# Performance work log

Measured on AMD Instinct MI355X. Metric: run time of the kernel, lower is better.

## Reference

```python
import jax, jax.numpy as jnp
import numpy as np

VOC, EMB, HID = 32000, 512, 1024
B, S = 16, 256


def setup_inputs() -> dict:
    key = jax.random.key(0)
    ks = jax.random.split(key, 12)
    s_e = 1.0 / np.sqrt(HID)
    inp = {
        "inputs": jax.random.randint(ks[0], (B, S), 0, VOC, dtype=jnp.int64),
        "emb": jax.random.normal(ks[1], (VOC, EMB), dtype=jnp.float32),
        "W_ih1": jax.random.uniform(ks[2], (4 * HID, EMB), minval=-s_e, maxval=s_e),
        "W_hh1": jax.random.uniform(ks[3], (4 * HID, HID), minval=-s_e, maxval=s_e),
        "b_ih1": jax.random.uniform(ks[4], (4 * HID,), minval=-s_e, maxval=s_e),
        "b_hh1": jax.random.uniform(ks[5], (4 * HID,), minval=-s_e, maxval=s_e),
        "W_ih2": jax.random.uniform(ks[6], (4 * HID, HID), minval=-s_e, maxval=s_e),
        "W_hh2": jax.random.uniform(ks[7], (4 * HID, HID), minval=-s_e, maxval=s_e),
        "b_ih2": jax.random.uniform(ks[8], (4 * HID,), minval=-s_e, maxval=s_e),
        "b_hh2": jax.random.uniform(ks[9], (4 * HID,), minval=-s_e, maxval=s_e),
        "W_log": jax.random.uniform(ks[10], (VOC, HID), minval=-s_e, maxval=s_e),
        "b_log": jnp.zeros((VOC,), dtype=jnp.float32),  # init_weights zeroes logits bias
    }
    return inp


def _lstm_cell(x, h, c, W_ih, W_hh, b_ih, b_hh):
    # PyTorch LSTMCell: gates ordered (i, f, g, o)
    g = x @ W_ih.T + b_ih + h @ W_hh.T + b_hh  # [B, 4H]
    i, f, gg, o = jnp.split(g, 4, axis=-1)
    c_new = jax.nn.sigmoid(f) * c + jax.nn.sigmoid(i) * jnp.tanh(gg)
    h_new = jax.nn.sigmoid(o) * jnp.tanh(c_new)
    return h_new, c_new


def reference(inputs, emb, W_ih1, W_hh1, b_ih1, b_hh1,
              W_ih2, W_hh2, b_ih2, b_hh2, W_log, b_log):
    # Dropout is evaluated in inference mode (identity), for determinism.
    embed = emb[inputs]  # [B, S, E]
    xs = jnp.swapaxes(embed, 0, 1)  # [S, B, E]
    bsz = inputs.shape[0]
    h1 = jnp.zeros((bsz, HID), embed.dtype)
    c1 = jnp.zeros((bsz, HID), embed.dtype)
    h2 = jnp.zeros((bsz, HID), embed.dtype)
    c2 = jnp.zeros((bsz, HID), embed.dtype)

    def step(carry, x_t):
        h1, c1, h2, c2 = carry
        h1, c1 = _lstm_cell(x_t, h1, c1, W_ih1, W_hh1, b_ih1, b_hh1)
        h2, c2 = _lstm_cell(h1, h2, c2, W_ih2, W_hh2, b_ih2, b_hh2)
        return (h1, c1, h2, c2), h2

    _, hid_seq = jax.lax.scan(step, (h1, c1, h2, c2), xs)  # [S, B, H]
    hid_seq = jnp.swapaxes(hid_seq, 0, 1)  # [B, S, H]
    logits = hid_seq @ W_log.T + b_log  # [B, S, V]
    return jax.nn.log_softmax(logits, axis=-1)
```

## Files before the change

kernel.cpp:

```cpp
#include <hip/hip_runtime.h>
#include <hip/hip_bf16.h>

typedef __attribute__((ext_vector_type(8))) _Float16 half8;
typedef __attribute__((ext_vector_type(4))) _Float16 half4;
typedef __attribute__((ext_vector_type(4))) float f32x4;
typedef __attribute__((ext_vector_type(4))) unsigned int u32x4;

#define VOC 32000
#define EMB 512
#define HID 1024
#define SS  256
#define NROW 4096
#define CHK 43
#define CSTRIDE 64
#define SLOTB (64 * CSTRIDE * 16)
#define NS 4
#define SPIN (1 << 16)
#define ROWH 264

__device__ __forceinline__ float sigf(float x) {
    return 1.f / (1.f + __expf(-x));
}
__device__ __forceinline__ float tanh_c(float x) {
    x = fminf(fmaxf(x, -15.f), 15.f);
    float e = __expf(2.f * x);
    return (e - 1.f) / (e + 1.f);
}

__device__ __forceinline__ u32x4 ldg_u4_cc(const void* p) {
    u32x4 r;
    asm volatile("global_load_dwordx4 %0, %1, off sc0 sc1" : "=v"(r) : "v"(p));
    return r;
}
__device__ __forceinline__ void stg_u4_cc(void* p, u32x4 v) {
    asm volatile("global_store_dwordx4 %0, %1, off sc0 sc1" :: "v"(p), "v"(v) : "memory");
}
__device__ __forceinline__ void stg_u32_cc(unsigned* p, unsigned v) {
    asm volatile("global_store_dword %0, %1, off sc0 sc1" :: "v"(p), "v"(v) : "memory");
}
__device__ __forceinline__ unsigned ldg_u32_cc(const unsigned* p) {
    unsigned v;
    asm volatile("global_load_dword %0, %1, off sc0 sc1\n\ts_waitcnt vmcnt(0)"
                 : "=v"(v) : "v"(p) : "memory");
    return v;
}
__device__ __forceinline__ half8 to_agpr(half8 v) {
    asm volatile("" : "+a"(v));
    return v;
}
__device__ __forceinline__ void gload16(const void* g, void* lds) {
    __builtin_amdgcn_global_load_lds(
        (const __attribute__((address_space(1))) unsigned int*)(uintptr_t)g,
        (__attribute__((address_space(3))) unsigned int*)(unsigned int)(uintptr_t)lds,
        16, 0, 0);
}

__global__ void k_zero(float* p, int n) {
    int i = blockIdx.x * blockDim.x + threadIdx.x;
    int st = gridDim.x * blockDim.x;
    for (; i < n; i += st) p[i] = 0.f;
}

__global__ void k_cvt_all(const float* __restrict__ s0, const float* __restrict__ s1,
                          const float* __restrict__ s2, const float* __restrict__ s3,
                          const float* __restrict__ s4,
                          _Float16* __restrict__ d0, _Float16* __restrict__ d1,
                          _Float16* __restrict__ d2, _Float16* __restrict__ d3,
                          _Float16* __restrict__ d4) {
    const int n0 = 4096 * 512 / 4;
    const int n1 = 4096 * 1024 / 4;
    const int n4 = VOC * 1024 / 4;
    const int nT = n0 + 3 * n1 + n4;
    int i = blockIdx.x * 256 + threadIdx.x;
    int st = gridDim.x * 256;
    for (; i < nT; i += st) {
        const float* s; _Float16* d; int k = i;
        if (k < n0) { s = s0; d = d0; }
        else {
            k -= n0;
            if (k < n1) { s = s1; d = d1; }
            else {
                k -= n1;
                if (k < n1) { s = s2; d = d2; }
                else {
                    k -= n1;
                    if (k < n1) { s = s3; d = d3; }
                    else { k -= n1; s = s4; d = d4; }
                }
            }
        }
        float4 v = ((const float4*)s)[k];
        half4 o = {(_Float16)v.x, (_Float16)v.y, (_Float16)v.z, (_Float16)v.w};
        ((half4*)d)[k] = o;
    }
}

__global__ void k_bias(const float* bi1, const float* bh1,
                       const float* bi2, const float* bh2,
                       float* b1, float* b2) {
    int i = blockIdx.x * blockDim.x + threadIdx.x;
    if (i < 4 * HID) { b1[i] = bi1[i] + bh1[i]; b2[i] = bi2[i] + bh2[i]; }
}

__global__ void k_embed(const int* __restrict__ tok, const float* __restrict__ emb,
                        _Float16* __restrict__ A) {
    int idx = blockIdx.x * 256 + threadIdx.x;
    if (idx >= NROW * (EMB / 4)) return;
    int r = idx >> 7, c4 = idx & 127;
    int t = r >> 4, b = r & 15;
    int token = tok[b * SS + t];
    float4 v = ((const float4*)(emb + (size_t)token * EMB))[c4];
    half4 o = {(_Float16)v.x, (_Float16)v.y, (_Float16)v.z, (_Float16)v.w};
    ((half4*)(A + (size_t)r * EMB))[c4] = o;
}

template <int F16OUT>
__global__ __launch_bounds__(256) void k_gemm_bt(
    const _Float16* __restrict__ A, const _Float16* __restrict__ B,
    const float* __restrict__ bias, float* __restrict__ C,
    _Float16* __restrict__ Ch, int M, int N, int K, int scatter, int swz) {
    __shared__ __align__(16) _Float16 As[128 * 32];
    __shared__ __align__(16) _Float16 Bs[128 * 32];
    int tid = threadIdx.x;
    int wave = tid >> 6, lane = tid & 63;
    int nbx = gridDim.x;
    int lin = blockIdx.y * nbx + blockIdx.x;
    if (swz) {
        int n = nbx * gridDim.y, cpx = n >> 3;
        lin = (lin & 7) * cpx + (lin >> 3);
    }
    int bRow = (lin / nbx) * 128, bCol = (lin % nbx) * 128;
    int wr = (wave >> 1) * 64, wc = (wave & 1) * 64;
    f32x4 acc[4][4] = {};

    int lrow = lane & 15, khalf = (lane >> 4) * 8;

    for (int kt = 0; kt < K; kt += 32) {
#pragma unroll
        for (int q = 0; q < 2; ++q) {
            int ci = q * 256 + wave * 64 + lane;
            int row = ci >> 2, c8 = (ci & 3) * 8;
            int ldsoff = (q * 256 + wave * 64) * 16;
            gload16(A + (size_t)(bRow + row) * K + kt + c8, (char*)As + ldsoff);
            gload16(B + (size_t)(bCol + row) * K + kt + c8, (char*)Bs + ldsoff);
        }
        __syncthreads();
        half8 a[4], b[4];
#pragma unroll
        for (int i = 0; i < 4; ++i)
            a[i] = *(const half8*)(&As[(wr + 16 * i + lrow) * 32 + khalf]);
#pragma unroll
        for (int j = 0; j < 4; ++j)
            b[j] = *(const half8*)(&Bs[(wc + 16 * j + lrow) * 32 + khalf]);
#pragma unroll
        for (int i = 0; i < 4; ++i)
#pragma unroll
            for (int j = 0; j < 4; ++j)
                acc[i][j] = __builtin_amdgcn_mfma_f32_16x16x32_f16(a[i], b[j], acc[i][j], 0, 0, 0);
        __syncthreads();
    }

    int lcol = lane & 15, lrow4 = (lane >> 4) * 4;
#pragma unroll
    for (int i = 0; i < 4; ++i)
#pragma unroll
        for (int j = 0; j < 4; ++j)
#pragma unroll
            for (int q = 0; q < 4; ++q) {
                int gr = bRow + wr + 16 * i + lrow4 + q;
                int gc = bCol + wc + 16 * j + lcol;
                float v = acc[i][j][q] + bias[gc];
                size_t orow = scatter ? (size_t)(((gr & 15) << 8) | (gr >> 4)) : (size_t)gr;
                if (F16OUT) Ch[orow * (size_t)N + gc] = (_Float16)v;
                else        C[orow * (size_t)N + gc] = v;
            }
}

template <int F16OUT>
__global__ __launch_bounds__(512, 1) void k_gemm8(
    const _Float16* __restrict__ A, const _Float16* __restrict__ B,
    const float* __restrict__ bias, float* __restrict__ Cf,
    _Float16* __restrict__ Ch, int M, int N, int K, int scatter) {
    __shared__ __align__(16) char smem[131072];
    int tid = threadIdx.x;
    int wave = tid >> 6, lane = tid & 63;
    int wm = wave >> 2, wn = wave & 3;
    int nbx = gridDim.x;
    int lin = blockIdx.y * nbx + blockIdx.x;
    {
        int n = nbx * gridDim.y;
        if ((n & 7) == 0) { int cpx = n >> 3; lin = (lin & 7) * cpx + (lin >> 3); }
    }
    int bRow = (lin / nbx) * 256, bCol = (lin % nbx) * 256;
    int nt = K >> 6;
    int lrow = lane & 15, kq = lane >> 4;

    auto stage = [&](int mat, int h, int t) {
        const _Float16* src = mat ? B : A;
        int r0 = mat ? bCol : bRow;
        char* dst = smem + (size_t)(t & 1) * 65536 + mat * 32768 + h * 16384;
#pragma unroll
        for (int j = 0; j < 2; ++j) {
            int ci = j * 512 + tid;
            int row = ci >> 3, slot = ci & 7;
            int grow = h * 128 + row;
            int gsl = slot ^ (row & 7);
            gload16(src + (size_t)(r0 + grow) * K + t * 64 + gsl * 8, dst + ci * 16);
        }
    };
    auto rdA = [&](int bf, int mi, int kk) -> half8 {
        int r = wm * 128 + mi * 16 + lrow;
        int sl = (kk * 4 + kq) ^ (lrow & 7);
        return *(const half8*)(smem + (size_t)bf * 65536 + r * 128 + sl * 16);
    };
    auto rdB = [&](int bf, int ni, int kk) -> half8 {
        int r = wn * 64 + ni * 16 + lrow;
        int sl = (kk * 4 + kq) ^ (lrow & 7);
        return *(const half8*)(smem + (size_t)bf * 65536 + 32768 + r * 128 + sl * 16);
    };

    f32x4 acc[8][4] = {};

    stage(1, 0, 0); stage(0, 0, 0); stage(1, 1, 0); stage(0, 1, 0);
    if (nt > 1) { stage(1, 0, 1); stage(0, 0, 1); }

    for (int u = 0; u < nt; ++u) {
        int bf = u & 1;
        if (u + 1 == nt) asm volatile("s_waitcnt vmcnt(0)" ::: "memory");
        else             asm volatile("s_waitcnt vmcnt(4)" ::: "memory");
        __builtin_amdgcn_s_barrier();
        __builtin_amdgcn_sched_barrier(0);
        if (u + 1 < nt) stage(1, 1, u + 1);
        half8 a[8][2], b[4][2];
#pragma unroll
        for (int mi = 0; mi < 8; ++mi)
#pragma unroll
            for (int kk = 0; kk < 2; ++kk)
                a[mi][kk] = rdA(bf, mi, kk);
#pragma unroll
        for (int ni = 0; ni < 4; ++ni)
#pragma unroll
            for (int kk = 0; kk < 2; ++kk)
                b[ni][kk] = rdB(bf, ni, kk);
        __builtin_amdgcn_s_setprio(1);
#pragma unroll
        for (int mi = 0; mi < 8; ++mi)
#pragma unroll
            for (int ni = 0; ni < 4; ++ni) {
                acc[mi][ni] = __builtin_amdgcn_mfma_f32_16x16x32_f16(a[mi][0], b[ni][0], acc[mi][ni], 0, 0, 0);
                acc[mi][ni] = __builtin_amdgcn_mfma_f32_16x16x32_f16(a[mi][1], b[ni][1], acc[mi][ni], 0, 0, 0);
            }
        __builtin_amdgcn_s_setprio(0);
        asm volatile("s_waitcnt lgkmcnt(0)" ::: "memory");
        __builtin_amdgcn_s_barrier();
        __builtin_amdgcn_sched_barrier(0);
        if (u + 1 < nt) stage(0, 1, u + 1);
        if (u + 2 < nt) { stage(1, 0, u + 2); stage(0, 0, u + 2); }
    }

    float bv[4];
#pragma unroll
    for (int ni = 0; ni < 4; ++ni)
        bv[ni] = bias[bCol + wn * 64 + ni * 16 + lrow];
#pragma unroll
    for (int mi = 0; mi < 8; ++mi)
#pragma unroll
        for (int ni = 0; ni < 4; ++ni)
#pragma unroll
            for (int q = 0; q < 4; ++q) {
                int gr = bRow + wm * 128 + mi * 16 + kq * 4 + q;
                int gc = bCol + wn * 64 + ni * 16 + lrow;
                float v = acc[mi][ni][q] + bv[ni];
                size_t orow = scatter ? (size_t)(((gr & 15) << 8) | (gr >> 4)) : (size_t)gr;
                if (F16OUT) Ch[orow * (size_t)N + gc] = (_Float16)v;
                else        Cf[orow * (size_t)N + gc] = v;
            }
}

__device__ __forceinline__ void poll_stage2(const char* base, int exp, int cnt,
                                            unsigned short* hs, int sbp, int r) {
    u32x4 cv[11];
#pragma unroll
    for (int j = 0; j < 11; ++j)
        if (j < cnt) cv[j] = ldg_u4_cc(base + j * 64);
    for (int it = 0; it < SPIN; ++it) {
        asm volatile("s_waitcnt vmcnt(0)" ::: "memory");
        __builtin_amdgcn_sched_barrier(0);
        bool bad = false;
#pragma unroll
        for (int j = 0; j < 11; ++j)
            if (j < cnt && (int)cv[j][3] < exp) {
                cv[j] = ldg_u4_cc(base + j * 64);
                bad = true;
            }
        if (!bad) break;
        __builtin_amdgcn_s_sleep(1);
    }
#pragma unroll
    for (int j = 0; j < 11; ++j)
        if (j < cnt) {
            int c = r + 4 * j;
            unsigned* dst = (unsigned*)((char*)hs + sbp * (2 * ROWH) + c * 12);
            dst[0] = cv[j][0]; dst[1] = cv[j][1]; dst[2] = cv[j][2];
        }
}

__global__ __launch_bounds__(256, 1) void k_rnn(
    const _Float16* __restrict__ X,
    const _Float16* __restrict__ Whh1,
    const _Float16* __restrict__ Wih2,
    const _Float16* __restrict__ Whh2,
    const float* __restrict__ b2s,
    char* __restrict__ h1buf,
    char* __restrict__ h2buf,
    unsigned* __restrict__ prog,
    _Float16* __restrict__ h2seq) {
    __shared__ __align__(16) unsigned short hsPA[64 * ROWH];
    __shared__ __align__(16) unsigned short hsPB[64 * ROWH];
    __shared__ float gs[4][1024];
    __shared__ __align__(16) unsigned short hstage[264];
    int tid = threadIdx.x;
    int w = tid >> 6, l = tid & 63;
    int bid = blockIdx.x;
    int layer = bid >> 6, sb = bid & 63;
    int sbp = tid >> 2, r = tid & 3;
    int cnt = (r == 3) ? 10 : 11;
    size_t choff = (size_t)(sbp * CSTRIDE + r) * 16;
    int hp = l >> 5;
    int hoff = (l & 15) * 16 + ((l >> 4) & 1) * 8;

    half8 wA[32];
    half8 wB[32];
    {
        const _Float16* base = layer ? Wih2 : Whh1;
        const _Float16* wp = base + (size_t)(w * HID + sb * 16 + (l & 15)) * HID + (l >> 4) * 8;
#pragma unroll
        for (int kt = 0; kt < 32; ++kt)
            wA[kt] = to_agpr(*(const half8*)(wp + kt * 32));
        if (layer) {
            const _Float16* wq = Whh2 + (size_t)(w * HID + sb * 16 + (l & 15)) * HID + (l >> 4) * 8;
#pragma unroll
            for (int kt = 0; kt < 32; ++kt)
                wB[kt] = to_agpr(*(const half8*)(wq + kt * 32));
        }
    }
    float bias_v = layer ? b2s[w * HID + sb * 16 + (l & 15)] : 0.f;

    int eb = tid >> 4, ecol = tid & 15;
    int gidx = ((eb >> 2) * 16 + ecol) * 4 + (eb & 3);
    float creg = 0.f;
    int pc = 0;

    if (!layer) {
        const _Float16* xbase = X + (size_t)w * HID + sb * 16 + (l & 15);
        int bq = (l >> 4) * 4;
        f32x4 xreg;
        {
            const _Float16* xp = xbase + (size_t)bq * 4096;
            xreg[0] = (float)xp[0]; xreg[1] = (float)xp[4096];
            xreg[2] = (float)xp[8192]; xreg[3] = (float)xp[12288];
        }
        for (int g = 0; g < SS; ++g) {
            int tn = (g + 1 < SS) ? g + 1 : SS - 1;
            const _Float16* xp = xbase + (size_t)(tn * 16 + bq) * 4096;
            float xn0 = (float)xp[0], xn1 = (float)xp[4096],
                  xn2 = (float)xp[8192], xn3 = (float)xp[12288];

            poll_stage2(h1buf + ((g - 1) & 3) * SLOTB + choff, g, cnt, hsPA, sbp, r);
            __syncthreads();
            if (tid == 0) stg_u32_cc(prog + (size_t)bid * 16, (unsigned)(g + 1));

            f32x4 a0 = xreg, a1 = {}, a2 = {}, a3 = {};
#pragma unroll
            for (int c = 0; c < 4; ++c) {
                half8 ha[8];
#pragma unroll
                for (int j = 0; j < 8; ++j)
                    ha[j] = *(const half8*)(hsPA + (2 * (c * 8 + j) + hp) * ROWH + hoff);
#pragma unroll
                for (int j = 0; j < 8; ++j) {
                    f32x4* ac = (j & 3) == 0 ? &a0 : (j & 3) == 1 ? &a1 : (j & 3) == 2 ? &a2 : &a3;
                    *ac = __builtin_amdgcn_mfma_f32_16x16x32_f16(ha[j], wA[c * 8 + j], *ac, 0, 0, 0);
                }
            }
            a0 = (a0 + a1) + (a2 + a3);

            *(f32x4*)(&gs[w][l * 4]) = a0;
            __syncthreads();

            float gi = gs[0][gidx], gf = gs[1][gidx], gg = gs[2][gidx], go = gs[3][gidx];
            float cn = sigf(gf) * creg + sigf(gi) * tanh_c(gg);
            float hn = sigf(go) * tanh_c(cn);
            creg = cn;
            _Float16 hh = (_Float16)hn;
            unsigned short hu;
            __builtin_memcpy(&hu, &hh, 2);
            hstage[eb * 16 + ecol] = hu;
            xreg[0] = xn0; xreg[1] = xn1; xreg[2] = xn2; xreg[3] = xn3;
            __syncthreads();

            if (tid < 128 && pc < g - 2) {
                const unsigned* pp = prog + (size_t)tid * 16;
                for (int it = 0; it < SPIN; ++it) {
                    unsigned v = ldg_u32_cc(pp);
                    if ((int)v >= g - 2) { pc = (int)v; break; }
                    __builtin_amdgcn_s_sleep(1);
                }
            }
            __syncthreads();
            if (w == 0 && l < CHK) {
                const unsigned* hsu = (const unsigned*)hstage;
                u32x4 pv;
                pv[0] = hsu[l * 3]; pv[1] = hsu[l * 3 + 1]; pv[2] = hsu[l * 3 + 2];
                pv[3] = (unsigned)(g + 1);
                stg_u4_cc(h1buf + (g & 3) * SLOTB + (size_t)(sb * CSTRIDE + l) * 16, pv);
            }
        }
    } else {
        for (int s = 0; s < SS; ++s) {
            poll_stage2(h2buf + ((s - 1) & 3) * SLOTB + choff, s, cnt, hsPB, sbp, r);
            poll_stage2(h1buf + (s & 3) * SLOTB + choff, s + 1, cnt, hsPA, sbp, r);
            __syncthreads();
            if (tid == 0) stg_u32_cc(prog + (size_t)bid * 16, (unsigned)(s + 1));

            f32x4 a0 = {bias_v, bias_v, bias_v, bias_v}, a1 = {}, a2 = {}, a3 = {};
#pragma unroll
            for (int c = 0; c < 4; ++c) {
                half8 ha[8];
#pragma unroll
                for (int j = 0; j < 8; ++j)
                    ha[j] = *(const half8*)(hsPB + (2 * (c * 8 + j) + hp) * ROWH + hoff);
#pragma unroll
                for (int j = 0; j < 8; ++j) {
                    f32x4* ac = (j & 3) == 0 ? &a0 : (j & 3) == 1 ? &a1 : (j & 3) == 2 ? &a2 : &a3;
                    *ac = __builtin_amdgcn_mfma_f32_16x16x32_f16(ha[j], wB[c * 8 + j], *ac, 0, 0, 0);
                }
            }
#pragma unroll
            for (int c = 0; c < 4; ++c) {
                half8 ha[8];
#pragma unroll
                for (int j = 0; j < 8; ++j)
                    ha[j] = *(const half8*)(hsPA + (2 * (c * 8 + j) + hp) * ROWH + hoff);
#pragma unroll
                for (int j = 0; j < 8; ++j) {
                    f32x4* ac = (j & 3) == 0 ? &a0 : (j & 3) == 1 ? &a1 : (j & 3) == 2 ? &a2 : &a3;
                    *ac = __builtin_amdgcn_mfma_f32_16x16x32_f16(ha[j], wA[c * 8 + j], *ac, 0, 0, 0);
                }
            }
            a0 = (a0 + a1) + (a2 + a3);

            *(f32x4*)(&gs[w][l * 4]) = a0;
            __syncthreads();

            float gi = gs[0][gidx], gf = gs[1][gidx], gg = gs[2][gidx], go = gs[3][gidx];
            float cn = sigf(gf) * creg + sigf(gi) * tanh_c(gg);
            float hn = sigf(go) * tanh_c(cn);
            creg = cn;
            _Float16 hh = (_Float16)hn;
            unsigned short hu;
            __builtin_memcpy(&hu, &hh, 2);
            hstage[eb * 16 + ecol] = hu;
            __syncthreads();

            if (tid < 64 && pc < s - 2) {
                const unsigned* pp = prog + (size_t)(64 + tid) * 16;
                for (int it = 0; it < SPIN; ++it) {
                    unsigned v = ldg_u32_cc(pp);
                    if ((int)v >= s - 2) { pc = (int)v; break; }
                    __builtin_amdgcn_s_sleep(1);
                }
            }
            __syncthreads();
            if (w == 0 && l < CHK) {
                const unsigned* hsu = (const unsigned*)hstage;
                u32x4 pv;
                pv[0] = hsu[l * 3]; pv[1] = hsu[l * 3 + 1]; pv[2] = hsu[l * 3 + 2];
                pv[3] = (unsigned)(s + 1);
                stg_u4_cc(h2buf + (s & 3) * SLOTB + (size_t)(sb * CSTRIDE + l) * 16, pv);
            }
            if (w == 1 && l < 32) {
                half8 hv = *(const half8*)((const char*)hstage + l * 16);
                *(half8*)(h2seq + (size_t)(s * 16 + (l >> 1)) * HID + sb * 16 + (l & 1) * 8) = hv;
            }
        }
    }
}

__global__ __launch_bounds__(320) void k_lsm_f(float* __restrict__ logits) {
    int r = blockIdx.x, tid = threadIdx.x;
    float* row = logits + (size_t)r * VOC;
    f32x4 v[25];
    float m = -3.4e38f;
#pragma unroll
    for (int j = 0; j < 25; ++j) {
        v[j] = ((const f32x4*)row)[tid + 320 * j];
        m = fmaxf(fmaxf(fmaxf(m, v[j][0]), fmaxf(v[j][1], v[j][2])), v[j][3]);
    }
#pragma unroll
    for (int off = 1; off < 64; off <<= 1) m = fmaxf(m, __shfl_xor(m, off));
    __shared__ float sm[5], ssum[5];
    int wv = tid >> 6;
    if ((tid & 63) == 0) sm[wv] = m;
    __syncthreads();
    m = fmaxf(fmaxf(fmaxf(sm[0], sm[1]), fmaxf(sm[2], sm[3])), sm[4]);
    float s = 0.f;
#pragma unroll
    for (int j = 0; j < 25; ++j)
        s += (__expf(v[j][0] - m) + __expf(v[j][1] - m)) +
             (__expf(v[j][2] - m) + __expf(v[j][3] - m));
#pragma unroll
    for (int off = 1; off < 64; off <<= 1) s += __shfl_xor(s, off);
    if ((tid & 63) == 0) ssum[wv] = s;
    __syncthreads();
    s = (ssum[0] + ssum[1]) + (ssum[2] + ssum[3]) + ssum[4];
    float lse = m + __logf(s);
#pragma unroll
    for (int j = 0; j < 25; ++j) {
        f32x4 o = v[j];
        o[0] -= lse; o[1] -= lse; o[2] -= lse; o[3] -= lse;
        ((f32x4*)row)[tid + 320 * j] = o;
    }
}

__global__ __launch_bounds__(320) void k_lsm_h(const _Float16* __restrict__ lg,
                                               float* __restrict__ out) {
    int r = blockIdx.x, tid = threadIdx.x;
    const half4* row = (const half4*)(lg + (size_t)r * VOC);
    float* orow = out + (size_t)r * VOC;
    half4 v[25];
    float m = -3.4e38f;
#pragma unroll
    for (int j = 0; j < 25; ++j) {
        v[j] = row[tid + 320 * j];
        float a = (float)v[j][0], b = (float)v[j][1], c = (float)v[j][2], d = (float)v[j][3];
        m = fmaxf(fmaxf(fmaxf(m, a), fmaxf(b, c)), d);
    }
#pragma unroll
    for (int off = 1; off < 64; off <<= 1) m = fmaxf(m, __shfl_xor(m, off));
    __shared__ float sm[5], ssum[5];
    int wv = tid >> 6;
    if ((tid & 63) == 0) sm[wv] = m;
    __syncthreads();
    m = fmaxf(fmaxf(fmaxf(sm[0], sm[1]), fmaxf(sm[2], sm[3])), sm[4]);
    float s = 0.f;
#pragma unroll
    for (int j = 0; j < 25; ++j)
        s += (__expf((float)v[j][0] - m) + __expf((float)v[j][1] - m)) +
             (__expf((float)v[j][2] - m) + __expf((float)v[j][3] - m));
#pragma unroll
    for (int off = 1; off < 64; off <<= 1) s += __shfl_xor(s, off);
    if ((tid & 63) == 0) ssum[wv] = s;
    __syncthreads();
    s = (ssum[0] + ssum[1]) + (ssum[2] + ssum[3]) + ssum[4];
    float lse = m + __logf(s);
#pragma unroll
    for (int j = 0; j < 25; ++j) {
        f32x4 o = {(float)v[j][0] - lse, (float)v[j][1] - lse,
                   (float)v[j][2] - lse, (float)v[j][3] - lse};
        ((f32x4*)orow)[tid + 320 * j] = o;
    }
}

extern "C" void kernel_launch(void* const* d_in, const int* in_sizes, int n_in,
                              void* d_out, int out_size, void* d_ws, size_t ws_size,
                              hipStream_t stream) {
    const int*   tok   = (const int*)d_in[0];
    const float* emb   = (const float*)d_in[1];
    const float* W_ih1 = (const float*)d_in[2];
    const float* W_hh1 = (const float*)d_in[3];
    const float* b_ih1 = (const float*)d_in[4];
    const float* b_hh1 = (const float*)d_in[5];
    const float* W_ih2 = (const float*)d_in[6];
    const float* W_hh2 = (const float*)d_in[7];
    const float* b_ih2 = (const float*)d_in[8];
    const float* b_hh2 = (const float*)d_in[9];
    const float* W_log = (const float*)d_in[10];
    const float* b_log = (const float*)d_in[11];
    float* out = (float*)d_out;

    char* w = (char*)d_ws;
    auto alloc = [&](size_t bytes) {
        char* p = w;
        w += (bytes + 255) & ~(size_t)255;
        return p;
    };
    _Float16* Wih1h = (_Float16*)alloc((size_t)4096 * 512 * 2);
    _Float16* Whh1h = (_Float16*)alloc((size_t)4096 * 1024 * 2);
    _Float16* Wih2h = (_Float16*)alloc((size_t)4096 * 1024 * 2);
    _Float16* Whh2h = (_Float16*)alloc((size_t)4096 * 1024 * 2);
    _Float16* Wlogh = (_Float16*)alloc((size_t)VOC * 1024 * 2);
    _Float16* Abuf  = (_Float16*)alloc((size_t)4096 * 512 * 2);
    _Float16* Xh    = (_Float16*)alloc((size_t)4096 * 4096 * 2);
    _Float16* h2seq = (_Float16*)alloc((size_t)4096 * 1024 * 2);
    float* b1s      = (float*)alloc(4096 * 4);
    float* b2s      = (float*)alloc(4096 * 4);
    char* h1buf     = alloc(NS * SLOTB);
    char* h2buf     = alloc(NS * SLOTB);
    unsigned* prog  = (unsigned*)alloc(128 * 64);
    size_t need = (size_t)(w - (char*)d_ws) + (size_t)NROW * VOC * 2;
    _Float16* logh = (need <= ws_size) ? (_Float16*)alloc((size_t)NROW * VOC * 2) : nullptr;

    k_zero<<<64, 256, 0, stream>>>((float*)h1buf, (2 * NS * SLOTB + 128 * 64) / 4);

    k_cvt_all<<<2048, 256, 0, stream>>>(W_ih1, W_hh1, W_ih2, W_hh2, W_log,
                                        Wih1h, Whh1h, Wih2h, Whh2h, Wlogh);
    k_bias<<<16, 256, 0, stream>>>(b_ih1, b_hh1, b_ih2, b_hh2, b1s, b2s);

    k_embed<<<2048, 256, 0, stream>>>(tok, emb, Abuf);
    k_gemm_bt<1><<<dim3(32, 32), 256, 0, stream>>>(Abuf, Wih1h, b1s, nullptr, Xh,
                                                   4096, 4096, 512, 0, 1);

    k_rnn<<<128, 256, 0, stream>>>(Xh, Whh1h, Wih2h, Whh2h, b2s,
                                   h1buf, h2buf, prog, h2seq);

    if (logh) {
        k_gemm8<1><<<dim3(VOC / 256, 16), 512, 0, stream>>>(h2seq, Wlogh, b_log,
                                                            nullptr, logh,
                                                            4096, VOC, 1024, 1);
        k_lsm_h<<<4096, 320, 0, stream>>>(logh, out);
    } else {
        k_gemm8<0><<<dim3(VOC / 256, 16), 512, 0, stream>>>(h2seq, Wlogh, b_log,
                                                            out, nullptr,
                                                            4096, VOC, 1024, 1);
        k_lsm_f<<<4096, 320, 0, stream>>>(out);
    }
}
```

Before: 1.600 ms.

## Overlap layer-2 h1 polling with h2 MFMAs and reuse large GEMM for input projection

In the layer-2 recurrent loop, loads for both the previous h2 chunk and the current h1 chunk are issued together. The h2 contribution is computed first, and the h1 tags are checked and staged only after those MFMAs, so waiting on layer 1 overlaps with compute. The progress flag is now published after h1 staging. The input-projection GEMM switches from the 128x128 tile kernel to the 256x256 k_gemm8 kernel, and the old kernel is deleted. This adds an extra barrier per step and depends on the vmcnt(10) count matching the number of loads in flight.

```diff
diff --git a/kernel.cpp b/kernel.cpp
--- a/kernel.cpp
+++ b/kernel.cpp
@@ -115,68 +115,6 @@
 }
 
 template <int F16OUT>
-__global__ __launch_bounds__(256) void k_gemm_bt(
-    const _Float16* __restrict__ A, const _Float16* __restrict__ B,
-    const float* __restrict__ bias, float* __restrict__ C,
-    _Float16* __restrict__ Ch, int M, int N, int K, int scatter, int swz) {
-    __shared__ __align__(16) _Float16 As[128 * 32];
-    __shared__ __align__(16) _Float16 Bs[128 * 32];
-    int tid = threadIdx.x;
-    int wave = tid >> 6, lane = tid & 63;
-    int nbx = gridDim.x;
-    int lin = blockIdx.y * nbx + blockIdx.x;
-    if (swz) {
-        int n = nbx * gridDim.y, cpx = n >> 3;
-        lin = (lin & 7) * cpx + (lin >> 3);
-    }
-    int bRow = (lin / nbx) * 128, bCol = (lin % nbx) * 128;
-    int wr = (wave >> 1) * 64, wc = (wave & 1) * 64;
-    f32x4 acc[4][4] = {};
-
-    int lrow = lane & 15, khalf = (lane >> 4) * 8;
-
-    for (int kt = 0; kt < K; kt += 32) {
-#pragma unroll
-        for (int q = 0; q < 2; ++q) {
-            int ci = q * 256 + wave * 64 + lane;
-            int row = ci >> 2, c8 = (ci & 3) * 8;
-            int ldsoff = (q * 256 + wave * 64) * 16;
-            gload16(A + (size_t)(bRow + row) * K + kt + c8, (char*)As + ldsoff);
-            gload16(B + (size_t)(bCol + row) * K + kt + c8, (char*)Bs + ldsoff);
-        }
-        __syncthreads();
-        half8 a[4], b[4];
-#pragma unroll
-        for (int i = 0; i < 4; ++i)
-            a[i] = *(const half8*)(&As[(wr + 16 * i + lrow) * 32 + khalf]);
-#pragma unroll
-        for (int j = 0; j < 4; ++j)
-            b[j] = *(const half8*)(&Bs[(wc + 16 * j + lrow) * 32 + khalf]);
-#pragma unroll
-        for (int i = 0; i < 4; ++i)
-#pragma unroll
-            for (int j = 0; j < 4; ++j)
-                acc[i][j] = __builtin_amdgcn_mfma_f32_16x16x32_f16(a[i], b[j], acc[i][j], 0, 0, 0);
-        __syncthreads();
-    }
-
-    int lcol = lane & 15, lrow4 = (lane >> 4) * 4;
-#pragma unroll
-    for (int i = 0; i < 4; ++i)
-#pragma unroll
-        for (int j = 0; j < 4; ++j)
-#pragma unroll
-            for (int q = 0; q < 4; ++q) {
-                int gr = bRow + wr + 16 * i + lrow4 + q;
-                int gc = bCol + wc + 16 * j + lcol;
-                float v = acc[i][j][q] + bias[gc];
-                size_t orow = scatter ? (size_t)(((gr & 15) << 8) | (gr >> 4)) : (size_t)gr;
-                if (F16OUT) Ch[orow * (size_t)N + gc] = (_Float16)v;
-                else        C[orow * (size_t)N + gc] = v;
-            }
-}
-
-template <int F16OUT>
 __global__ __launch_bounds__(512, 1) void k_gemm8(
     const _Float16* __restrict__ A, const _Float16* __restrict__ B,
     const float* __restrict__ bias, float* __restrict__ Cf,
@@ -277,15 +215,20 @@
             }
 }
 
-__device__ __forceinline__ void poll_stage2(const char* base, int exp, int cnt,
-                                            unsigned short* hs, int sbp, int r) {
-    u32x4 cv[11];
+__device__ __forceinline__ void poll_issue(const char* base, int cnt, u32x4* cv) {
 #pragma unroll
     for (int j = 0; j < 11; ++j)
         if (j < cnt) cv[j] = ldg_u4_cc(base + j * 64);
+}
+__device__ __forceinline__ bool tags_ok(const u32x4* cv, int exp, int cnt) {
+    bool ok = true;
+#pragma unroll
+    for (int j = 0; j < 11; ++j)
+        if (j < cnt && (int)cv[j][3] < exp) ok = false;
+    return ok;
+}
+__device__ __forceinline__ void poll_retry(const char* base, int exp, int cnt, u32x4* cv) {
     for (int it = 0; it < SPIN; ++it) {
-        asm volatile("s_waitcnt vmcnt(0)" ::: "memory");
-        __builtin_amdgcn_sched_barrier(0);
         bool bad = false;
 #pragma unroll
         for (int j = 0; j < 11; ++j)
@@ -295,7 +238,12 @@
             }
         if (!bad) break;
         __builtin_amdgcn_s_sleep(1);
-    }
+        asm volatile("s_waitcnt vmcnt(0)" ::: "memory");
+        __builtin_amdgcn_sched_barrier(0);
+    }
+}
+__device__ __forceinline__ void stage_cv(const u32x4* cv, unsigned short* hs,
+                                         int sbp, int r, int cnt) {
 #pragma unroll
     for (int j = 0; j < 11; ++j)
         if (j < cnt) {
@@ -303,6 +251,15 @@
             unsigned* dst = (unsigned*)((char*)hs + sbp * (2 * ROWH) + c * 12);
             dst[0] = cv[j][0]; dst[1] = cv[j][1]; dst[2] = cv[j][2];
         }
+}
+__device__ __forceinline__ void poll_stage2(const char* base, int exp, int cnt,
+                                            unsigned short* hs, int sbp, int r) {
+    u32x4 cv[11];
+    poll_issue(base, cnt, cv);
+    asm volatile("s_waitcnt vmcnt(0)" ::: "memory");
+    __builtin_amdgcn_sched_barrier(0);
+    poll_retry(base, exp, cnt, cv);
+    stage_cv(cv, hs, sbp, r, cnt);
 }
 
 __global__ __launch_bounds__(256, 1) void k_rnn(
@@ -418,10 +375,20 @@
         }
     } else {
         for (int s = 0; s < SS; ++s) {
-            poll_stage2(h2buf + ((s - 1) & 3) * SLOTB + choff, s, cnt, hsPB, sbp, r);
-            poll_stage2(h1buf + (s & 3) * SLOTB + choff, s + 1, cnt, hsPA, sbp, r);
-            __syncthreads();
-            if (tid == 0) stg_u32_cc(prog + (size_t)bid * 16, (unsigned)(s + 1));
+            const char* baseB = h2buf + ((s - 1) & 3) * SLOTB + choff;
+            const char* baseA = h1buf + (s & 3) * SLOTB + choff;
+            u32x4 cvB[11], cvA[11];
+            poll_issue(baseB, cnt, cvB);
+            poll_issue(baseA, cnt, cvA);
+            asm volatile("s_waitcnt vmcnt(10)" ::: "memory");
+            __builtin_amdgcn_sched_barrier(0);
+            if (!tags_ok(cvB, s, cnt)) {
+                asm volatile("s_waitcnt vmcnt(0)" ::: "memory");
+                __builtin_amdgcn_sched_barrier(0);
+                poll_retry(baseB, s, cnt, cvB);
+            }
+            stage_cv(cvB, hsPB, sbp, r, cnt);
+            __syncthreads();
 
             f32x4 a0 = {bias_v, bias_v, bias_v, bias_v}, a1 = {}, a2 = {}, a3 = {};
 #pragma unroll
@@ -436,6 +403,13 @@
                     *ac = __builtin_amdgcn_mfma_f32_16x16x32_f16(ha[j], wB[c * 8 + j], *ac, 0, 0, 0);
                 }
             }
+            asm volatile("s_waitcnt vmcnt(0)" ::: "memory");
+            __builtin_amdgcn_sched_barrier(0);
+            if (!tags_ok(cvA, s + 1, cnt)) poll_retry(baseA, s + 1, cnt, cvA);
+            stage_cv(cvA, hsPA, sbp, r, cnt);
+            __syncthreads();
+            if (tid == 0) stg_u32_cc(prog + (size_t)bid * 16, (unsigned)(s + 1));
+
 #pragma unroll
             for (int c = 0; c < 4; ++c) {
                 half8 ha[8];
@@ -608,8 +582,8 @@
     k_bias<<<16, 256, 0, stream>>>(b_ih1, b_hh1, b_ih2, b_hh2, b1s, b2s);
 
     k_embed<<<2048, 256, 0, stream>>>(tok, emb, Abuf);
-    k_gemm_bt<1><<<dim3(32, 32), 256, 0, stream>>>(Abuf, Wih1h, b1s, nullptr, Xh,
-                                                   4096, 4096, 512, 0, 1);
+    k_gemm8<1><<<dim3(16, 16), 512, 0, stream>>>(Abuf, Wih1h, b1s, nullptr, Xh,
+                                                 4096, 4096, 512, 0);
 
     k_rnn<<<128, 256, 0, stream>>>(Xh, Whh1h, Wih2h, Whh2h, b2s,
                                    h1buf, h2buf, prog, h2seq);
```

Result: slower. 1.710 ms (+6.9%).

## Overlap logits GEMM with LSTM recurrence using extra spin-waiting blocks

Applied to the files above, without the earlier changes.

Launches 128 extra blocks alongside the 128 persistent LSTM blocks. The extra blocks poll the layer-2 progress counters and compute logits tiles for finished timestep rows while the recurrence is still running. The remaining columns and rows are covered afterwards by offset launches of the large GEMM. The input-projection GEMM also switches from the 128-tile kernel to the 256-tile kernel, and h2seq stores now bypass cache so the concurrent consumers see them. The cost is that the extra blocks compete with the recurrence for CUs and memory bandwidth, and the scheme depends on all blocks being co-resident to avoid deadlock.

```diff
diff --git a/kernel.cpp b/kernel.cpp
--- a/kernel.cpp
+++ b/kernel.cpp
@@ -17,6 +17,8 @@
 #define NS 4
 #define SPIN (1 << 16)
 #define ROWH 264
+#define SH_TR 30
+#define SH_TC 150
 
 __device__ __forceinline__ float sigf(float x) {
     return 1.f / (1.f + __expf(-x));
@@ -33,6 +35,9 @@
     return r;
 }
 __device__ __forceinline__ void stg_u4_cc(void* p, u32x4 v) {
+    asm volatile("global_store_dwordx4 %0, %1, off sc0 sc1" :: "v"(p), "v"(v) : "memory");
+}
+__device__ __forceinline__ void stg_h8_cc(_Float16* p, half8 v) {
     asm volatile("global_store_dwordx4 %0, %1, off sc0 sc1" :: "v"(p), "v"(v) : "memory");
 }
 __device__ __forceinline__ void stg_u32_cc(unsigned* p, unsigned v) {
@@ -115,72 +120,11 @@
 }
 
 template <int F16OUT>
-__global__ __launch_bounds__(256) void k_gemm_bt(
-    const _Float16* __restrict__ A, const _Float16* __restrict__ B,
-    const float* __restrict__ bias, float* __restrict__ C,
-    _Float16* __restrict__ Ch, int M, int N, int K, int scatter, int swz) {
-    __shared__ __align__(16) _Float16 As[128 * 32];
-    __shared__ __align__(16) _Float16 Bs[128 * 32];
-    int tid = threadIdx.x;
-    int wave = tid >> 6, lane = tid & 63;
-    int nbx = gridDim.x;
-    int lin = blockIdx.y * nbx + blockIdx.x;
-    if (swz) {
-        int n = nbx * gridDim.y, cpx = n >> 3;
-        lin = (lin & 7) * cpx + (lin >> 3);
-    }
-    int bRow = (lin / nbx) * 128, bCol = (lin % nbx) * 128;
-    int wr = (wave >> 1) * 64, wc = (wave & 1) * 64;
-    f32x4 acc[4][4] = {};
-
-    int lrow = lane & 15, khalf = (lane >> 4) * 8;
-
-    for (int kt = 0; kt < K; kt += 32) {
-#pragma unroll
-        for (int q = 0; q < 2; ++q) {
-            int ci = q * 256 + wave * 64 + lane;
-            int row = ci >> 2, c8 = (ci & 3) * 8;
-            int ldsoff = (q * 256 + wave * 64) * 16;
-            gload16(A + (size_t)(bRow + row) * K + kt + c8, (char*)As + ldsoff);
-            gload16(B + (size_t)(bCol + row) * K + kt + c8, (char*)Bs + ldsoff);
-        }
-        __syncthreads();
-        half8 a[4], b[4];
-#pragma unroll
-        for (int i = 0; i < 4; ++i)
-            a[i] = *(const half8*)(&As[(wr + 16 * i + lrow) * 32 + khalf]);
-#pragma unroll
-        for (int j = 0; j < 4; ++j)
-            b[j] = *(const half8*)(&Bs[(wc + 16 * j + lrow) * 32 + khalf]);
-#pragma unroll
-        for (int i = 0; i < 4; ++i)
-#pragma unroll
-            for (int j = 0; j < 4; ++j)
-                acc[i][j] = __builtin_amdgcn_mfma_f32_16x16x32_f16(a[i], b[j], acc[i][j], 0, 0, 0);
-        __syncthreads();
-    }
-
-    int lcol = lane & 15, lrow4 = (lane >> 4) * 4;
-#pragma unroll
-    for (int i = 0; i < 4; ++i)
-#pragma unroll
-        for (int j = 0; j < 4; ++j)
-#pragma unroll
-            for (int q = 0; q < 4; ++q) {
-                int gr = bRow + wr + 16 * i + lrow4 + q;
-                int gc = bCol + wc + 16 * j + lcol;
-                float v = acc[i][j][q] + bias[gc];
-                size_t orow = scatter ? (size_t)(((gr & 15) << 8) | (gr >> 4)) : (size_t)gr;
-                if (F16OUT) Ch[orow * (size_t)N + gc] = (_Float16)v;
-                else        C[orow * (size_t)N + gc] = v;
-            }
-}
-
-template <int F16OUT>
 __global__ __launch_bounds__(512, 1) void k_gemm8(
     const _Float16* __restrict__ A, const _Float16* __restrict__ B,
     const float* __restrict__ bias, float* __restrict__ Cf,
-    _Float16* __restrict__ Ch, int M, int N, int K, int scatter) {
+    _Float16* __restrict__ Ch, int M, int N, int K, int scatter,
+    int rowOff, int colOff) {
     __shared__ __align__(16) char smem[131072];
     int tid = threadIdx.x;
     int wave = tid >> 6, lane = tid & 63;
@@ -191,7 +135,7 @@
         int n = nbx * gridDim.y;
         if ((n & 7) == 0) { int cpx = n >> 3; lin = (lin & 7) * cpx + (lin >> 3); }
     }
-    int bRow = (lin / nbx) * 256, bCol = (lin % nbx) * 256;
+    int bRow = rowOff + (lin / nbx) * 256, bCol = colOff + (lin % nbx) * 256;
     int nt = K >> 6;
     int lrow = lane & 15, kq = lane >> 4;
 
@@ -305,23 +249,87 @@
         }
 }
 
-__global__ __launch_bounds__(256, 1) void k_rnn(
+__global__ __launch_bounds__(256, 1) void k_fused(
     const _Float16* __restrict__ X,
-    const _Float16* __restrict__ Whh1,
-    const _Float16* __restrict__ Wih2,
-    const _Float16* __restrict__ Whh2,
-    const float* __restrict__ b2s,
-    char* __restrict__ h1buf,
-    char* __restrict__ h2buf,
-    unsigned* __restrict__ prog,
-    _Float16* __restrict__ h2seq) {
-    __shared__ __align__(16) unsigned short hsPA[64 * ROWH];
-    __shared__ __align__(16) unsigned short hsPB[64 * ROWH];
-    __shared__ float gs[4][1024];
-    __shared__ __align__(16) unsigned short hstage[264];
+    const _Float16* __restrict__ Whh1, const _Float16* __restrict__ Wih2,
+    const _Float16* __restrict__ Whh2, const float* __restrict__ b2s,
+    char* __restrict__ h1buf, char* __restrict__ h2buf,
+    unsigned* __restrict__ prog, _Float16* __restrict__ h2seq,
+    const _Float16* __restrict__ Wlog, const float* __restrict__ blog,
+    _Float16* __restrict__ logh) {
+    __shared__ __align__(16) char smem[84992];
     int tid = threadIdx.x;
+    int bid = blockIdx.x;
+
+    if (bid >= 128) {
+        _Float16* As = (_Float16*)smem;
+        _Float16* Bs = (_Float16*)(smem + 8192);
+        int wave = tid >> 6, lane = tid & 63;
+        int wr = (wave >> 1) * 64, wc = (wave & 1) * 64;
+        int lrow = lane & 15, khalf = (lane >> 4) * 8;
+        int lcol = lane & 15, lrow4 = (lane >> 4) * 4;
+        int pcg = -1;
+        for (int idx = bid - 128; idx < SH_TR * SH_TC; idx += 128) {
+            int tr = idx / SH_TC, tc = idx % SH_TC;
+            int needed = tr * 8 + 12;
+            if (pcg < needed) {
+                if (tid < 64) {
+                    const unsigned* pp = prog + (size_t)(64 + tid) * 16;
+                    for (int it = 0; it < SPIN; ++it) {
+                        unsigned v = ldg_u32_cc(pp);
+                        if ((int)v >= needed) break;
+                        __builtin_amdgcn_s_sleep(16);
+                    }
+                }
+                __syncthreads();
+                pcg = needed;
+            }
+            int bRow = tr * 128, bCol = tc * 128;
+            f32x4 acc[4][4] = {};
+            for (int kt = 0; kt < HID; kt += 32) {
+#pragma unroll
+                for (int q = 0; q < 2; ++q) {
+                    int ci = q * 256 + wave * 64 + lane;
+                    int row = ci >> 2, c8 = (ci & 3) * 8;
+                    int ldsoff = (q * 256 + wave * 64) * 16;
+                    gload16(h2seq + (size_t)(bRow + row) * HID + kt + c8, (char*)As + ldsoff);
+                    gload16(Wlog + (size_t)(bCol + row) * HID + kt + c8, (char*)Bs + ldsoff);
+                }
+                __syncthreads();
+                half8 a[4], b[4];
+#pragma unroll
+                for (int i = 0; i < 4; ++i)
+                    a[i] = *(const half8*)(&As[(wr + 16 * i + lrow) * 32 + khalf]);
+#pragma unroll
+                for (int j = 0; j < 4; ++j)
+                    b[j] = *(const half8*)(&Bs[(wc + 16 * j + lrow) * 32 + khalf]);
+#pragma unroll
+                for (int i = 0; i < 4; ++i)
+#pragma unroll
+                    for (int j = 0; j < 4; ++j)
+                        acc[i][j] = __builtin_amdgcn_mfma_f32_16x16x32_f16(a[i], b[j], acc[i][j], 0, 0, 0);
+                __syncthreads();
+            }
+#pragma unroll
+            for (int i = 0; i < 4; ++i)
+#pragma unroll
+                for (int j = 0; j < 4; ++j)
+#pragma unroll
+                    for (int q = 0; q < 4; ++q) {
+                        int gr = bRow + wr + 16 * i + lrow4 + q;
+                        int gc = bCol + wc + 16 * j + lcol;
+                        size_t orow = (size_t)(((gr & 15) << 8) | (gr >> 4));
+                        logh[orow * (size_t)VOC + gc] = (_Float16)(acc[i][j][q] + blog[gc]);
+                    }
+        }
+        return;
+    }
+
+    unsigned short* hsPA = (unsigned short*)smem;
+    unsigned short* hsPB = (unsigned short*)(smem + 33792);
+    float* gsp = (float*)(smem + 67584);
+    unsigned short* hstage = (unsigned short*)(smem + 83968);
     int w = tid >> 6, l = tid & 63;
-    int bid = blockIdx.x;
     int layer = bid >> 6, sb = bid & 63;
     int sbp = tid >> 2, r = tid & 3;
     int cnt = (r == 3) ? 10 : 11;
@@ -385,10 +393,11 @@
             }
             a0 = (a0 + a1) + (a2 + a3);
 
-            *(f32x4*)(&gs[w][l * 4]) = a0;
-            __syncthreads();
-
-            float gi = gs[0][gidx], gf = gs[1][gidx], gg = gs[2][gidx], go = gs[3][gidx];
+            *(f32x4*)(&gsp[w * 1024 + l * 4]) = a0;
+            __syncthreads();
+
+            float gi = gsp[gidx], gf = gsp[1024 + gidx],
+                  gg = gsp[2048 + gidx], go = gsp[3072 + gidx];
             float cn = sigf(gf) * creg + sigf(gi) * tanh_c(gg);
             float hn = sigf(go) * tanh_c(cn);
             creg = cn;
@@ -450,10 +459,11 @@
             }
             a0 = (a0 + a1) + (a2 + a3);
 
-            *(f32x4*)(&gs[w][l * 4]) = a0;
-            __syncthreads();
-
-            float gi = gs[0][gidx], gf = gs[1][gidx], gg = gs[2][gidx], go = gs[3][gidx];
+            *(f32x4*)(&gsp[w * 1024 + l * 4]) = a0;
+            __syncthreads();
+
+            float gi = gsp[gidx], gf = gsp[1024 + gidx],
+                  gg = gsp[2048 + gidx], go = gsp[3072 + gidx];
             float cn = sigf(gf) * creg + sigf(gi) * tanh_c(gg);
             float hn = sigf(go) * tanh_c(cn);
             creg = cn;
@@ -481,7 +491,7 @@
             }
             if (w == 1 && l < 32) {
                 half8 hv = *(const half8*)((const char*)hstage + l * 16);
-                *(half8*)(h2seq + (size_t)(s * 16 + (l >> 1)) * HID + sb * 16 + (l & 1) * 8) = hv;
+                stg_h8_cc(h2seq + (size_t)(s * 16 + (l >> 1)) * HID + sb * 16 + (l & 1) * 8, hv);
             }
         }
     }
@@ -608,21 +618,27 @@
     k_bias<<<16, 256, 0, stream>>>(b_ih1, b_hh1, b_ih2, b_hh2, b1s, b2s);
 
     k_embed<<<2048, 256, 0, stream>>>(tok, emb, Abuf);
-    k_gemm_bt<1><<<dim3(32, 32), 256, 0, stream>>>(Abuf, Wih1h, b1s, nullptr, Xh,
-                                                   4096, 4096, 512, 0, 1);
-
-    k_rnn<<<128, 256, 0, stream>>>(Xh, Whh1h, Wih2h, Whh2h, b2s,
-                                   h1buf, h2buf, prog, h2seq);
+    k_gemm8<1><<<dim3(16, 16), 512, 0, stream>>>(Abuf, Wih1h, b1s, nullptr, Xh,
+                                                 4096, 4096, 512, 0, 0, 0);
 
     if (logh) {
-        k_gemm8<1><<<dim3(VOC / 256, 16), 512, 0, stream>>>(h2seq, Wlogh, b_log,
-                                                            nullptr, logh,
-                                                            4096, VOC, 1024, 1);
+        k_fused<<<256, 256, 0, stream>>>(Xh, Whh1h, Wih2h, Whh2h, b2s,
+                                         h1buf, h2buf, prog, h2seq,
+                                         Wlogh, b_log, logh);
+        k_gemm8<1><<<dim3(50, 16), 512, 0, stream>>>(h2seq, Wlogh, b_log, nullptr,
+                                                     logh, 4096, VOC, 1024, 1,
+                                                     0, 19200);
+        k_gemm8<1><<<dim3(75, 1), 512, 0, stream>>>(h2seq, Wlogh, b_log, nullptr,
+                                                    logh, 4096, VOC, 1024, 1,
+                                                    3840, 0);
         k_lsm_h<<<4096, 320, 0, stream>>>(logh, out);
     } else {
+        k_fused<<<128, 256, 0, stream>>>(Xh, Whh1h, Wih2h, Whh2h, b2s,
+                                         h1buf, h2buf, prog, h2seq,
+                                         Wlogh, b_log, nullptr);
         k_gemm8<0><<<dim3(VOC / 256, 16), 512, 0, stream>>>(h2seq, Wlogh, b_log,
                                                             out, nullptr,
-                                                            4096, VOC, 1024, 1);
+                                                            4096, VOC, 1024, 1, 0, 0);
         k_lsm_f<<<4096, 320, 0, stream>>>(out);
     }
 }
```

New measurement: 1.532 ms. -4.2%, faster.
